# Kernel tuning notes

Measured on AMD Instinct MI355X. Metric: run time of the kernel, lower is better.

The kernel has to match this reference:

```python
import jax, jax.numpy as jnp
import numpy as np

N = 50000      # note nodes
IN = 128       # input feature dim
HID = 256      # GNN hidden dim
OH = 128       # hidden_dim // 2 after gnn.lin
CH = 64        # clf hidden (OH // 2)
OUT = 7        # cadence classes
E = 500000     # edges per relation
L = 3          # num_layers
T = 4          # edge types: onset, consecutive, during, rest
EPS = 1e-5


def _layernorm(h, g, b):
    mu = h.mean(-1, keepdims=True)
    var = h.var(-1, keepdims=True)
    return (h - mu) * jax.lax.rsqrt(var + EPS) * g + b


def setup_inputs() -> dict:
    key = jax.random.key(0)
    ks = jax.random.split(key, 24)
    s = 0.05
    inp = {
        "x": jax.random.normal(ks[0], (N, IN), jnp.float32),
        "edge_onset": jax.random.randint(ks[1], (2, E), 0, N),
        "edge_consecutive": jax.random.randint(ks[2], (2, E), 0, N),
        "edge_during": jax.random.randint(ks[3], (2, E), 0, N),
        "edge_rest": jax.random.randint(ks[4], (2, E), 0, N),
        # SAGEConv params: lin_l (with bias) on aggregated neighbors, lin_r (no bias) on self
        "Wl0": jax.random.normal(ks[5], (T, IN, HID), jnp.float32) * s,
        "bl0": jnp.zeros((T, HID), jnp.float32),
        "Wr0": jax.random.normal(ks[6], (T, IN, HID), jnp.float32) * s,
        "Wl": jax.random.normal(ks[7], (L - 1, T, HID, HID), jnp.float32) * s,
        "bl": jnp.zeros((L - 1, T, HID), jnp.float32),
        "Wr": jax.random.normal(ks[8], (L - 1, T, HID, HID), jnp.float32) * s,
        "lin_W": jax.random.normal(ks[9], (HID, OH), jnp.float32) * s,
        "lin_b": jnp.zeros((OH,), jnp.float32),
        "norm_g": jnp.ones((OH,), jnp.float32),
        "norm_b": jnp.zeros((OH,), jnp.float32),
        "pW1": jax.random.normal(ks[10], (OH, OH), jnp.float32) * s,
        "pb1": jnp.zeros((OH,), jnp.float32),
        "pln_g": jnp.ones((OH,), jnp.float32),
        "pln_b": jnp.zeros((OH,), jnp.float32),
        "pW2": jax.random.normal(ks[11], (OH, OH), jnp.float32) * s,
        "pb2": jnp.zeros((OH,), jnp.float32),
        "cW1": jax.random.normal(ks[12], (OH, CH), jnp.float32) * s,
        "cb1": jnp.zeros((CH,), jnp.float32),
        "bn_g": jnp.ones((CH,), jnp.float32),
        "bn_b": jnp.zeros((CH,), jnp.float32),
        "cW2": jax.random.normal(ks[13], (CH, OUT), jnp.float32) * s,
        "cb2": jnp.zeros((OUT,), jnp.float32),
    }
    return inp


def _mean_aggr(h, e):
    # SAGEConv mean aggregation: mean of source features per destination node
    src, dst = e[0], e[1]
    s = jax.ops.segment_sum(h[src], dst, num_segments=N)
    c = jax.ops.segment_sum(jnp.ones((e.shape[1], 1), h.dtype), dst, num_segments=N)
    return s / jnp.maximum(c, 1.0)


def _hetero_layer(h, edges, Wl_t, bl_t, Wr_t):
    # HeteroConv(aggr='sum'): sum SAGEConv outputs over edge types
    out = jnp.zeros((N, Wl_t.shape[-1]), h.dtype)
    for t in range(T):
        m = _mean_aggr(h, edges[t])
        out = out + m @ Wl_t[t] + bl_t[t] + h @ Wr_t[t]
    return jax.nn.relu(out)


def reference(x, edge_onset, edge_consecutive, edge_during, edge_rest,
              Wl0, bl0, Wr0, Wl, bl, Wr, lin_W, lin_b, norm_g, norm_b,
              pW1, pb1, pln_g, pln_b, pW2, pb2,
              cW1, cb1, bn_g, bn_b, cW2, cb2):
    edges = [edge_onset, edge_consecutive, edge_during, edge_rest]
    h = _hetero_layer(x, edges, Wl0, bl0, Wr0)
    for l in range(L - 1):
        h = _hetero_layer(h, edges, Wl[l], bl[l], Wr[l])
    h = h @ lin_W + lin_b  # [N, OH]

    # onset pooling: torch_scatter.scatter_mean(x[src], dst, out=x.clone())
    # -> (x + scatter_sum) / max(count, 1)
    src, dst = edge_onset[0], edge_onset[1]
    s = jax.ops.segment_sum(h[src], dst, num_segments=N)
    c = jax.ops.segment_sum(jnp.ones((E,), h.dtype), dst, num_segments=N)
    h = (h + s) / jnp.maximum(c, 1.0)[:, None]

    h = _layernorm(h, norm_g, norm_b)
    # pool_mlp (dropout = identity in eval)
    h = _layernorm(jax.nn.relu(h @ pW1 + pb1), pln_g, pln_b) @ pW2 + pb2
    # cad_clf: Linear -> ReLU -> BatchNorm1d (batch stats) -> Dropout(id) -> Linear
    z = jax.nn.relu(h @ cW1 + cb1)
    mu = z.mean(0)
    var = z.var(0)
    z = (z - mu) * jax.lax.rsqrt(var + EPS) * bn_g + bn_b
    logits = z @ cW2 + cb2
    return jax.nn.softmax(logits, axis=-1)
```

## Files before the change

### kernel.cpp

```cpp
#include <hip/hip_runtime.h>
#include <hip/hip_bf16.h>

#define NN    50000
#define ROWS  50048
#define DIN   128
#define DHID  256
#define DOH   128
#define DCH   64
#define DOUT  7
#define NE    500000
#define OFFS  50004
#define EPSV  1e-5f
#define LDAGG 1024

typedef unsigned int uint;
typedef unsigned short ushort;
using short8 = __attribute__((ext_vector_type(8))) short;
using f32x4  = __attribute__((ext_vector_type(4))) float;

__device__ inline float b2f(ushort u) {
    union { float f; uint i; } v; v.i = ((uint)u) << 16; return v.f;
}
__device__ inline ushort f2b(float f) {
    union { float f; uint u; } v; v.f = f;
    uint r = v.u + 0x7fff + ((v.u >> 16) & 1);
    return (ushort)(r >> 16);
}


__global__ void count_k(const int* __restrict__ d0, const int* __restrict__ d1,
                        const int* __restrict__ d2, const int* __restrict__ d3,
                        int* __restrict__ cnt) {
    int i = blockIdx.x * blockDim.x + threadIdx.x;
    if (i >= NE) return;
    int t = blockIdx.y;
    const int* d = (t == 0) ? d0 : (t == 1) ? d1 : (t == 2) ? d2 : d3;
    atomicAdd(&cnt[t * NN + d[i]], 1);
}

__global__ __launch_bounds__(1024)
void scan_k(const int* __restrict__ cnt, int* __restrict__ off) {
    const int* c = cnt + blockIdx.x * NN;
    int* o = off + blockIdx.x * OFFS;
    __shared__ int wsums[16];
    int lane = threadIdx.x & 63, wid = threadIdx.x >> 6;
    int carry = 0;
    for (int base = 0; base < NN; base += 1024) {
        int i = base + threadIdx.x;
        int v = (i < NN) ? c[i] : 0;
        int x = v;
        #pragma unroll
        for (int s = 1; s < 64; s <<= 1) {
            int t = __shfl_up(x, s);
            if (lane >= s) x += t;
        }
        if (lane == 63) wsums[wid] = x;
        __syncthreads();
        if (wid == 0) {
            int wv = (lane < 16) ? wsums[lane] : 0;
            #pragma unroll
            for (int s = 1; s < 16; s <<= 1) {
                int t = __shfl_up(wv, s);
                if (lane >= s) wv += t;
            }
            if (lane < 16) wsums[lane] = wv;
        }
        __syncthreads();
        int wprev = (wid == 0) ? 0 : wsums[wid - 1];
        if (i < NN) o[i] = carry + wprev + x - v;
        carry += wsums[15];
        __syncthreads();
    }
    if (threadIdx.x == 0) o[NN] = carry;
}

__global__ void copyoff_k(const int* __restrict__ off, int* __restrict__ cursor) {
    int i = blockIdx.x * blockDim.x + threadIdx.x;
    int t = blockIdx.y;
    if (i < NN) cursor[t * NN + i] = off[t * OFFS + i];
}

__global__ void scatter_k(const int* __restrict__ e0, const int* __restrict__ e1,
                          const int* __restrict__ e2, const int* __restrict__ e3,
                          int* __restrict__ cursor, int* __restrict__ sorted) {
    int i = blockIdx.x * blockDim.x + threadIdx.x;
    if (i >= NE) return;
    int t = blockIdx.y;
    const int* e = (t == 0) ? e0 : (t == 1) ? e1 : (t == 2) ? e2 : e3;
    int src = e[i], dst = e[NE + i];
    int p = atomicAdd(&cursor[t * NN + dst], 1);
    sorted[t * NE + p] = src;
}


__global__ void wprep_layer_k(const float* __restrict__ Wl, const float* __restrict__ Wr,
                              ushort* __restrict__ Bt, int Din) {
    int KA = 5 * Din;
    int K2 = 2 * KA;
    int i = blockIdx.x * 256 + threadIdx.x;
    if (i >= 256 * KA) return;
    int n = i / KA, k = i - n * KA;
    float v;
    if (k < 4 * Din) {
        int t = k / Din, c = k - t * Din;
        v = Wl[((size_t)t * Din + c) * 256 + n];
    } else {
        int c = k - 4 * Din;
        v = Wr[(size_t)c * 256 + n] + Wr[((size_t)Din + c) * 256 + n]
          + Wr[((size_t)2 * Din + c) * 256 + n] + Wr[((size_t)3 * Din + c) * 256 + n];
    }
    ushort hi = f2b(v);
    Bt[(size_t)n * K2 + k] = hi;
    Bt[(size_t)n * K2 + KA + k] = f2b(v - b2f(hi));
}

__global__ void wprep_t3_k(const float* __restrict__ W, ushort* __restrict__ Bt,
                           int N, int K) {
    int K3 = 3 * K;
    int i = blockIdx.x * 256 + threadIdx.x;
    if (i >= N * K3) return;
    int n = i / K3, k3 = i - n * K3;
    int k = (k3 < K) ? k3 : ((k3 < 2 * K) ? k3 - K : k3 - 2 * K);
    float v = W[(size_t)k * N + n];
    ushort hi = f2b(v);
    Bt[i] = (k3 < 2 * K) ? hi : f2b(v - b2f(hi));
}

__global__ void wsum_k(const float* __restrict__ W, float* __restrict__ wsum, int KN) {
    int i = blockIdx.x * blockDim.x + threadIdx.x;
    if (i < KN) wsum[i] = W[i] + W[KN + i] + W[2 * KN + i] + W[3 * KN + i];
}

__global__ void xconv_k(const float* __restrict__ x, ushort* __restrict__ aggbuf) {
    int i = blockIdx.x * 256 + threadIdx.x;
    if (i >= NN * DIN) return;
    int node = i >> 7, c = i & 127;
    aggbuf[(size_t)node * LDAGG + 512 + c] = f2b(x[i]);
}


template <int VE>
__global__ __launch_bounds__(256)
void aggrb_k(const ushort* __restrict__ hsrc, int hstride,
             const int* __restrict__ off, const int* __restrict__ sorted,
             ushort* __restrict__ out, int ostride) {
    int node = blockIdx.x * 4 + (threadIdx.x >> 6);
    if (node >= NN) return;
    int t = blockIdx.y;
    int l = threadIdx.x & 63;
    const int* of = off + (size_t)t * OFFS;
    const int* so = sorted + (size_t)t * NE;
    int s0 = of[node], s1 = of[node + 1];
    const ushort* hb = hsrc + (size_t)l * VE;
    float a0[VE] = {}, a1[VE] = {}, a2[VE] = {}, a3[VE] = {};
    int e = s0;
    if (VE == 2) {
        for (; e + 4 <= s1; e += 4) {
            uint vA = *(const uint*)(hb + (size_t)so[e]     * hstride);
            uint vB = *(const uint*)(hb + (size_t)so[e + 1] * hstride);
            uint vC = *(const uint*)(hb + (size_t)so[e + 2] * hstride);
            uint vD = *(const uint*)(hb + (size_t)so[e + 3] * hstride);
            a0[0] += b2f((ushort)vA); a0[1] += b2f((ushort)(vA >> 16));
            a1[0] += b2f((ushort)vB); a1[1] += b2f((ushort)(vB >> 16));
            a2[0] += b2f((ushort)vC); a2[1] += b2f((ushort)(vC >> 16));
            a3[0] += b2f((ushort)vD); a3[1] += b2f((ushort)(vD >> 16));
        }
        for (; e < s1; ++e) {
            uint v = *(const uint*)(hb + (size_t)so[e] * hstride);
            a0[0] += b2f((ushort)v); a0[1] += b2f((ushort)(v >> 16));
        }
    } else {
        for (; e + 4 <= s1; e += 4) {
            uint2 vA = *(const uint2*)(hb + (size_t)so[e]     * hstride);
            uint2 vB = *(const uint2*)(hb + (size_t)so[e + 1] * hstride);
            uint2 vC = *(const uint2*)(hb + (size_t)so[e + 2] * hstride);
            uint2 vD = *(const uint2*)(hb + (size_t)so[e + 3] * hstride);
            a0[0] += b2f((ushort)vA.x); a0[1] += b2f((ushort)(vA.x >> 16));
            a0[2] += b2f((ushort)vA.y); a0[3] += b2f((ushort)(vA.y >> 16));
            a1[0] += b2f((ushort)vB.x); a1[1] += b2f((ushort)(vB.x >> 16));
            a1[2] += b2f((ushort)vB.y); a1[3] += b2f((ushort)(vB.y >> 16));
            a2[0] += b2f((ushort)vC.x); a2[1] += b2f((ushort)(vC.x >> 16));
            a2[2] += b2f((ushort)vC.y); a2[3] += b2f((ushort)(vC.y >> 16));
            a3[0] += b2f((ushort)vD.x); a3[1] += b2f((ushort)(vD.x >> 16));
            a3[2] += b2f((ushort)vD.y); a3[3] += b2f((ushort)(vD.y >> 16));
        }
        for (; e < s1; ++e) {
            uint2 v = *(const uint2*)(hb + (size_t)so[e] * hstride);
            a0[0] += b2f((ushort)v.x); a0[1] += b2f((ushort)(v.x >> 16));
            a0[2] += b2f((ushort)v.y); a0[3] += b2f((ushort)(v.y >> 16));
        }
    }
    int deg = s1 - s0;
    float inv = 1.f / (float)(deg > 0 ? deg : 1);
    ushort* orow = out + (size_t)node * ostride + t * (64 * VE) + l * VE;
    if (VE == 2) {
        float r0 = (a0[0] + a1[0] + a2[0] + a3[0]) * inv;
        float r1 = (a0[1] + a1[1] + a2[1] + a3[1]) * inv;
        *(uint*)orow = (uint)f2b(r0) | ((uint)f2b(r1) << 16);
    } else {
        uint2 o;
        float r0 = (a0[0] + a1[0] + a2[0] + a3[0]) * inv;
        float r1 = (a0[1] + a1[1] + a2[1] + a3[1]) * inv;
        float r2 = (a0[2] + a1[2] + a2[2] + a3[2]) * inv;
        float r3 = (a0[3] + a1[3] + a2[3] + a3[3]) * inv;
        o.x = (uint)f2b(r0) | ((uint)f2b(r1) << 16);
        o.y = (uint)f2b(r2) | ((uint)f2b(r3) << 16);
        *(uint2*)orow = o;
    }
}


template <int BN, int NWN, bool RELU, int OMODE>
__global__ __launch_bounds__(128 * NWN)
void mgemm_k(const ushort* __restrict__ A, int lda,
             const ushort* __restrict__ A2, int lda2, int ksplit,
             const ushort* __restrict__ Bt, const float* __restrict__ bias,
             void* __restrict__ Cout, int ldc, int M, int K2, int KA) {
    constexpr int T = 128 * NWN;
    __shared__ ushort lsA[128 * 40];
    __shared__ ushort lsB[BN * 40];
    const int tid = threadIdx.x;
    const int l = tid & 63, wid = tid >> 6;
    const int wm = wid / NWN, wn = wid % NWN;
    const int row0 = blockIdx.x * 128;
    f32x4 acc[4][4] = {};
    for (int k0 = 0; k0 < K2; k0 += 32) {
        int kA = (k0 < KA) ? k0 : k0 - KA;
        const ushort* srcA;
        int lsrc;
        if (kA < ksplit) { srcA = A + kA; lsrc = lda; }
        else             { srcA = A2 + (kA - ksplit); lsrc = lda2; }
        #pragma unroll
        for (int q = 0; q < 512 / T; ++q) {
            int ch = tid + q * T;
            int r = ch >> 2, cb = ch & 3;
            short8 v = *(const short8*)(srcA + (size_t)(row0 + r) * lsrc + cb * 8);
            *(short8*)(lsA + r * 40 + cb * 8) = v;
        }
        #pragma unroll
        for (int q = 0; q < BN * 4 / T; ++q) {
            int ch = tid + q * T;
            int r = ch >> 2, cb = ch & 3;
            short8 v = *(const short8*)(Bt + (size_t)r * K2 + k0 + cb * 8);
            *(short8*)(lsB + r * 40 + cb * 8) = v;
        }
        __syncthreads();
        short8 af[4], bfr[4];
        #pragma unroll
        for (int fm = 0; fm < 4; ++fm)
            af[fm] = *(const short8*)(lsA + (wm * 64 + fm * 16 + (l & 15)) * 40 + (l >> 4) * 8);
        #pragma unroll
        for (int fn = 0; fn < 4; ++fn)
            bfr[fn] = *(const short8*)(lsB + (wn * 64 + fn * 16 + (l & 15)) * 40 + (l >> 4) * 8);
        #pragma unroll
        for (int fm = 0; fm < 4; ++fm)
            #pragma unroll
            for (int fn = 0; fn < 4; ++fn)
                acc[fm][fn] = __builtin_amdgcn_mfma_f32_16x16x32_bf16(
                    af[fm], bfr[fn], acc[fm][fn], 0, 0, 0);
        __syncthreads();
    }
    #pragma unroll
    for (int fm = 0; fm < 4; ++fm) {
        #pragma unroll
        for (int fn = 0; fn < 4; ++fn) {
            int col = wn * 64 + fn * 16 + (l & 15);
            float bv = bias[col];
            #pragma unroll
            for (int q = 0; q < 4; ++q) {
                int row = row0 + wm * 64 + fm * 16 + (l >> 4) * 4 + q;
                if (row < M) {
                    float v = acc[fm][fn][q] + bv;
                    if (RELU) v = fmaxf(v, 0.f);
                    if (OMODE == 0) {
                        ((float*)Cout)[(size_t)row * ldc + col] = v;
                    } else if (OMODE == 1) {
                        ((ushort*)Cout)[(size_t)row * ldc + col] = f2b(v);
                    } else {
                        ushort hv = f2b(v);
                        ((ushort*)Cout)[(size_t)row * ldc + col] = hv;
                        ((ushort*)Cout)[(size_t)row * ldc + col + BN] = f2b(v - b2f(hv));
                    }
                }
            }
        }
    }
}


__device__ inline float waveReduceSum(float v) {
    #pragma unroll
    for (int s = 32; s > 0; s >>= 1) v += __shfl_xor(v, s);
    return v;
}

__global__ __launch_bounds__(256)
void poolln_k(const float* __restrict__ hL, const int* __restrict__ off,
              const int* __restrict__ sorted, const float* __restrict__ g,
              const float* __restrict__ b, ushort* __restrict__ outS) {
    int node = blockIdx.x * 4 + (threadIdx.x >> 6);
    if (node >= NN) return;
    int l = threadIdx.x & 63;
    int s0 = off[node], s1 = off[node + 1];
    const float* hb = hL + (size_t)l * 2;
    float2 self = *(const float2*)(hb + (size_t)node * DOH);
    float a00 = 0, a01 = 0, a10 = 0, a11 = 0, a20 = 0, a21 = 0, a30 = 0, a31 = 0;
    int e = s0;
    for (; e + 4 <= s1; e += 4) {
        float2 vA = *(const float2*)(hb + (size_t)sorted[e]     * DOH);
        float2 vB = *(const float2*)(hb + (size_t)sorted[e + 1] * DOH);
        float2 vC = *(const float2*)(hb + (size_t)sorted[e + 2] * DOH);
        float2 vD = *(const float2*)(hb + (size_t)sorted[e + 3] * DOH);
        a00 += vA.x; a01 += vA.y; a10 += vB.x; a11 += vB.y;
        a20 += vC.x; a21 += vC.y; a30 += vD.x; a31 += vD.y;
    }
    for (; e < s1; ++e) {
        float2 v = *(const float2*)(hb + (size_t)sorted[e] * DOH);
        a00 += v.x; a01 += v.y;
    }
    int deg = s1 - s0;
    float inv = 1.f / (float)(deg > 0 ? deg : 1);
    float v0 = (self.x + a00 + a10 + a20 + a30) * inv;
    float v1 = (self.y + a01 + a11 + a21 + a31) * inv;
    float mean = waveReduceSum(v0 + v1) * (1.f / DOH);
    float ex2  = waveReduceSum(v0 * v0 + v1 * v1) * (1.f / DOH);
    float rst = rsqrtf(ex2 - mean * mean + EPSV);
    float o0 = (v0 - mean) * rst * g[2 * l] + b[2 * l];
    float o1 = (v1 - mean) * rst * g[2 * l + 1] + b[2 * l + 1];
    ushort h0 = f2b(o0), h1 = f2b(o1);
    ushort l0 = f2b(o0 - b2f(h0)), l1 = f2b(o1 - b2f(h1));
    ushort* row = outS + (size_t)node * 256;
    *(uint*)(row + 2 * l)       = (uint)h0 | ((uint)h1 << 16);
    *(uint*)(row + 128 + 2 * l) = (uint)l0 | ((uint)l1 << 16);
}

__global__ __launch_bounds__(256)
void lns_k(ushort* __restrict__ hS, const float* __restrict__ g,
           const float* __restrict__ b) {
    int node = blockIdx.x * 4 + (threadIdx.x >> 6);
    if (node >= NN) return;
    int l = threadIdx.x & 63;
    ushort* row = hS + (size_t)node * 256;
    uint hh = *(uint*)(row + 2 * l);
    uint ll = *(uint*)(row + 128 + 2 * l);
    float v0 = b2f((ushort)hh) + b2f((ushort)ll);
    float v1 = b2f((ushort)(hh >> 16)) + b2f((ushort)(ll >> 16));
    float mean = waveReduceSum(v0 + v1) * (1.f / DOH);
    float ex2  = waveReduceSum(v0 * v0 + v1 * v1) * (1.f / DOH);
    float rst = rsqrtf(ex2 - mean * mean + EPSV);
    float o0 = (v0 - mean) * rst * g[2 * l] + b[2 * l];
    float o1 = (v1 - mean) * rst * g[2 * l + 1] + b[2 * l + 1];
    ushort h0 = f2b(o0), h1 = f2b(o1);
    ushort lo0 = f2b(o0 - b2f(h0)), lo1 = f2b(o1 - b2f(h1));
    *(uint*)(row + 2 * l)       = (uint)h0 | ((uint)h1 << 16);
    *(uint*)(row + 128 + 2 * l) = (uint)lo0 | ((uint)lo1 << 16);
}


__global__ __launch_bounds__(256)
void bnstat_k(const float* __restrict__ z, float* __restrict__ sums, int M) {
    int col = threadIdx.x & 63;
    int rgrp = threadIdx.x >> 6;
    float s = 0.f, s2 = 0.f;
    for (int r = blockIdx.x * 4 + rgrp; r < M; r += gridDim.x * 4) {
        float v = z[(size_t)r * DCH + col];
        s += v; s2 += v * v;
    }
    __shared__ float sh[2][4][64];
    sh[0][rgrp][col] = s;
    sh[1][rgrp][col] = s2;
    __syncthreads();
    if (rgrp == 0) {
        s  = sh[0][0][col] + sh[0][1][col] + sh[0][2][col] + sh[0][3][col];
        s2 = sh[1][0][col] + sh[1][1][col] + sh[1][2][col] + sh[1][3][col];
        atomicAdd(&sums[col], s);
        atomicAdd(&sums[64 + col], s2);
    }
}

__global__ __launch_bounds__(256)
void final_k(const float* __restrict__ z, const float* __restrict__ sums,
             const float* __restrict__ bn_g, const float* __restrict__ bn_b,
             const float* __restrict__ cW2, const float* __restrict__ cb2,
             float* __restrict__ out, int M) {
    int row = blockIdx.x * 4 + (threadIdx.x >> 6);
    int lane = threadIdx.x & 63;
    if (row >= M) return;
    float zv = z[(size_t)row * DCH + lane];
    float mean = sums[lane] * (1.f / M);
    float var = sums[64 + lane] * (1.f / M) - mean * mean;
    float zb = (zv - mean) * rsqrtf(var + EPSV) * bn_g[lane] + bn_b[lane];
    float logit[DOUT];
    #pragma unroll
    for (int o = 0; o < DOUT; ++o) {
        float p = zb * cW2[lane * DOUT + o];
        #pragma unroll
        for (int s = 32; s > 0; s >>= 1) p += __shfl_xor(p, s);
        logit[o] = p + cb2[o];
    }
    float mx = logit[0];
    #pragma unroll
    for (int o = 1; o < DOUT; ++o) mx = fmaxf(mx, logit[o]);
    float den = 0.f;
    #pragma unroll
    for (int o = 0; o < DOUT; ++o) { logit[o] = expf(logit[o] - mx); den += logit[o]; }
    float inv = 1.f / den;
    if (lane == 0) {
        #pragma unroll
        for (int o = 0; o < DOUT; ++o) out[(size_t)row * DOUT + o] = logit[o] * inv;
    }
}


extern "C" void kernel_launch(void* const* d_in, const int* in_sizes, int n_in,
                              void* d_out, int out_size, void* d_ws, size_t ws_size,
                              hipStream_t stream) {
    const float* x     = (const float*)d_in[0];
    const int* eptr[4] = {(const int*)d_in[1], (const int*)d_in[2],
                          (const int*)d_in[3], (const int*)d_in[4]};
    const float* Wl0   = (const float*)d_in[5];
    const float* bl0   = (const float*)d_in[6];
    const float* Wr0   = (const float*)d_in[7];
    const float* Wl    = (const float*)d_in[8];
    const float* bl    = (const float*)d_in[9];
    const float* Wr    = (const float*)d_in[10];
    const float* lin_W = (const float*)d_in[11];
    const float* lin_b = (const float*)d_in[12];
    const float* nrm_g = (const float*)d_in[13];
    const float* nrm_b = (const float*)d_in[14];
    const float* pW1   = (const float*)d_in[15];
    const float* pb1   = (const float*)d_in[16];
    const float* pln_g = (const float*)d_in[17];
    const float* pln_b = (const float*)d_in[18];
    const float* pW2   = (const float*)d_in[19];
    const float* pb2   = (const float*)d_in[20];
    const float* cW1   = (const float*)d_in[21];
    const float* cb1   = (const float*)d_in[22];
    const float* bn_g  = (const float*)d_in[23];
    const float* bn_b  = (const float*)d_in[24];
    const float* cW2   = (const float*)d_in[25];
    const float* cb2   = (const float*)d_in[26];

    size_t wo = 0;
    auto alloc = [&](size_t bytes) -> void* {
        void* p = (char*)d_ws + wo;
        wo += (bytes + 255) & ~(size_t)255;
        return p;
    };
    int* off      = (int*)alloc(4 * OFFS * sizeof(int));
    int* cursor   = (int*)alloc(4 * NN * sizeof(int));
    int* sorted   = (int*)alloc(4 * NE * sizeof(int));
    ushort* WBt   = (ushort*)alloc((size_t)256 * 2560 * 2);
    ushort* BtLin = (ushort*)alloc((size_t)128 * 768 * 2);
    ushort* BtP1  = (ushort*)alloc((size_t)128 * 384 * 2);
    ushort* BtP2  = (ushort*)alloc((size_t)128 * 384 * 2);
    ushort* BtC1  = (ushort*)alloc((size_t)64 * 384 * 2);
    float* bsum   = (float*)alloc(256 * sizeof(float));
    float* bnsum  = (float*)alloc(128 * sizeof(float));
    ushort* aggbuf = (ushort*)alloc((size_t)ROWS * LDAGG * 2);
    ushort* hc1   = (ushort*)alloc((size_t)ROWS * 256 * 2);
    ushort* hc2   = (ushort*)alloc((size_t)ROWS * 256 * 2);

    float*  hL  = (float*)hc1;
    ushort* hPs = hc2;
    ushort* hQs = aggbuf;
    ushort* hRs = (ushort*)((char*)aggbuf + ((size_t)32 << 20));
    float*  z   = (float*)((char*)aggbuf + ((size_t)64 << 20));

    const int EB = (NE + 255) / 256;
    const int GX = (NN + 127) / 128;
    const int AGG = (NN + 3) / 4;

    hipMemsetAsync(cursor, 0, 4 * NN * sizeof(int), stream);
    count_k<<<dim3(EB, 4), 256, 0, stream>>>(eptr[0] + NE, eptr[1] + NE,
                                             eptr[2] + NE, eptr[3] + NE, cursor);
    scan_k<<<4, 1024, 0, stream>>>(cursor, off);
    copyoff_k<<<dim3((NN + 255) / 256, 4), 256, 0, stream>>>(off, cursor);
    scatter_k<<<dim3(EB, 4), 256, 0, stream>>>(eptr[0], eptr[1], eptr[2], eptr[3],
                                               cursor, sorted);

    xconv_k<<<(NN * DIN + 255) / 256, 256, 0, stream>>>(x, aggbuf);

    wprep_layer_k<<<(256 * 640 + 255) / 256, 256, 0, stream>>>(Wl0, Wr0, WBt, DIN);
    wsum_k<<<1, 256, 0, stream>>>(bl0, bsum, DHID);
    aggrb_k<2><<<dim3(AGG, 4), 256, 0, stream>>>(aggbuf + 512, LDAGG, off, sorted,
                                                 aggbuf, LDAGG);
    mgemm_k<256, 4, true, 1><<<GX, 512, 0, stream>>>(
        aggbuf, LDAGG, aggbuf, LDAGG, 640, WBt, bsum, (void*)hc1, 256, NN, 1280, 640);

    for (int l = 1; l < 3; ++l) {
        const float* WlP = Wl + (size_t)(l - 1) * 4 * DHID * DHID;
        const float* blP = bl + (size_t)(l - 1) * 4 * DHID;
        const float* WrP = Wr + (size_t)(l - 1) * 4 * DHID * DHID;
        ushort* hin = (l == 1) ? hc1 : hc2;
        wprep_layer_k<<<(256 * 1280 + 255) / 256, 256, 0, stream>>>(WlP, WrP, WBt, DHID);
        wsum_k<<<1, 256, 0, stream>>>(blP, bsum, DHID);
        aggrb_k<4><<<dim3(AGG, 4), 256, 0, stream>>>(hin, 256, off, sorted,
                                                     aggbuf, LDAGG);
        if (l == 1)
            mgemm_k<256, 4, true, 1><<<GX, 512, 0, stream>>>(
                aggbuf, LDAGG, hin, 256, 1024, WBt, bsum, (void*)hc2, 256, NN, 2560, 1280);
        else
            mgemm_k<256, 4, true, 2><<<GX, 512, 0, stream>>>(
                aggbuf, LDAGG, hin, 256, 1024, WBt, bsum, (void*)aggbuf, LDAGG, NN, 2560, 1280);
    }

    wprep_t3_k<<<(128 * 768 + 255) / 256, 256, 0, stream>>>(lin_W, BtLin, DOH, DHID);
    mgemm_k<128, 2, false, 0><<<GX, 256, 0, stream>>>(
        aggbuf, LDAGG, aggbuf, LDAGG, 512, BtLin, lin_b, (void*)hL, DOH, NN, 768, 512);

    poolln_k<<<AGG, 256, 0, stream>>>(hL, off, sorted, nrm_g, nrm_b, hPs);

    wprep_t3_k<<<(128 * 384 + 255) / 256, 256, 0, stream>>>(pW1, BtP1, DOH, DOH);
    mgemm_k<128, 2, true, 2><<<GX, 256, 0, stream>>>(
        hPs, 256, hPs, 256, 256, BtP1, pb1, (void*)hQs, 256, NN, 384, 256);
    lns_k<<<AGG, 256, 0, stream>>>(hQs, pln_g, pln_b);
    wprep_t3_k<<<(128 * 384 + 255) / 256, 256, 0, stream>>>(pW2, BtP2, DOH, DOH);
    mgemm_k<128, 2, false, 2><<<GX, 256, 0, stream>>>(
        hQs, 256, hQs, 256, 256, BtP2, pb2, (void*)hRs, 256, NN, 384, 256);

    wprep_t3_k<<<(64 * 384 + 255) / 256, 256, 0, stream>>>(cW1, BtC1, DCH, DOH);
    mgemm_k<64, 1, true, 0><<<GX, 128, 0, stream>>>(
        hRs, 256, hRs, 256, 256, BtC1, cb1, (void*)z, DCH, NN, 384, 256);
    hipMemsetAsync(bnsum, 0, 128 * sizeof(float), stream);
    bnstat_k<<<256, 256, 0, stream>>>(z, bnsum, NN);
    final_k<<<AGG, 256, 0, stream>>>(z, bnsum, bn_g, bn_b, cW2, cb2,
                                     (float*)d_out, NN);
}
```

Before: 1.277 ms.

## Fuse neighbor mean aggregation into per-layer SAGE GEMM kernel and drop copyoff

Each of the three hetero SAGE layers now runs one kernel. It first gathers and averages neighbor features for its 128-row tile across all four relations into aggbuf, then runs the bf16 MFMA GEMM on those same rows. This removes a separate aggregation launch per layer and lets the GEMM read freshly written aggregates, likely from L2. The scan kernel also writes the cursor array directly, which removes the copyoff kernel. In exchange the gather phase no longer overlaps with the MFMA phase inside a block, and gather parallelism is now bound to the GEMM grid of large 512-thread blocks.

After: 1.521 ms. +19.1%, slower.

```diff
diff --git a/kernel.cpp b/kernel.cpp
--- a/kernel.cpp
+++ b/kernel.cpp
@@ -39,9 +39,11 @@
 }
 
 __global__ __launch_bounds__(1024)
-void scan_k(const int* __restrict__ cnt, int* __restrict__ off) {
+void scan_k(const int* __restrict__ cnt, int* __restrict__ off,
+            int* __restrict__ cursor) {
     const int* c = cnt + blockIdx.x * NN;
     int* o = off + blockIdx.x * OFFS;
+    int* cu = cursor + blockIdx.x * NN;
     __shared__ int wsums[16];
     int lane = threadIdx.x & 63, wid = threadIdx.x >> 6;
     int carry = 0;
@@ -67,17 +69,15 @@
         }
         __syncthreads();
         int wprev = (wid == 0) ? 0 : wsums[wid - 1];
-        if (i < NN) o[i] = carry + wprev + x - v;
+        if (i < NN) {
+            int ex = carry + wprev + x - v;
+            o[i] = ex;
+            cu[i] = ex;
+        }
         carry += wsums[15];
         __syncthreads();
     }
     if (threadIdx.x == 0) o[NN] = carry;
-}
-
-__global__ void copyoff_k(const int* __restrict__ off, int* __restrict__ cursor) {
-    int i = blockIdx.x * blockDim.x + threadIdx.x;
-    int t = blockIdx.y;
-    if (i < NN) cursor[t * NN + i] = off[t * OFFS + i];
 }
 
 __global__ void scatter_k(const int* __restrict__ e0, const int* __restrict__ e1,
@@ -139,73 +139,149 @@
 }
 
 
-template <int VE>
-__global__ __launch_bounds__(256)
-void aggrb_k(const ushort* __restrict__ hsrc, int hstride,
-             const int* __restrict__ off, const int* __restrict__ sorted,
-             ushort* __restrict__ out, int ostride) {
-    int node = blockIdx.x * 4 + (threadIdx.x >> 6);
-    if (node >= NN) return;
-    int t = blockIdx.y;
-    int l = threadIdx.x & 63;
-    const int* of = off + (size_t)t * OFFS;
-    const int* so = sorted + (size_t)t * NE;
-    int s0 = of[node], s1 = of[node + 1];
-    const ushort* hb = hsrc + (size_t)l * VE;
-    float a0[VE] = {}, a1[VE] = {}, a2[VE] = {}, a3[VE] = {};
-    int e = s0;
-    if (VE == 2) {
-        for (; e + 4 <= s1; e += 4) {
-            uint vA = *(const uint*)(hb + (size_t)so[e]     * hstride);
-            uint vB = *(const uint*)(hb + (size_t)so[e + 1] * hstride);
-            uint vC = *(const uint*)(hb + (size_t)so[e + 2] * hstride);
-            uint vD = *(const uint*)(hb + (size_t)so[e + 3] * hstride);
-            a0[0] += b2f((ushort)vA); a0[1] += b2f((ushort)(vA >> 16));
-            a1[0] += b2f((ushort)vB); a1[1] += b2f((ushort)(vB >> 16));
-            a2[0] += b2f((ushort)vC); a2[1] += b2f((ushort)(vC >> 16));
-            a3[0] += b2f((ushort)vD); a3[1] += b2f((ushort)(vD >> 16));
-        }
-        for (; e < s1; ++e) {
-            uint v = *(const uint*)(hb + (size_t)so[e] * hstride);
-            a0[0] += b2f((ushort)v); a0[1] += b2f((ushort)(v >> 16));
-        }
-    } else {
-        for (; e + 4 <= s1; e += 4) {
-            uint2 vA = *(const uint2*)(hb + (size_t)so[e]     * hstride);
-            uint2 vB = *(const uint2*)(hb + (size_t)so[e + 1] * hstride);
-            uint2 vC = *(const uint2*)(hb + (size_t)so[e + 2] * hstride);
-            uint2 vD = *(const uint2*)(hb + (size_t)so[e + 3] * hstride);
-            a0[0] += b2f((ushort)vA.x); a0[1] += b2f((ushort)(vA.x >> 16));
-            a0[2] += b2f((ushort)vA.y); a0[3] += b2f((ushort)(vA.y >> 16));
-            a1[0] += b2f((ushort)vB.x); a1[1] += b2f((ushort)(vB.x >> 16));
-            a1[2] += b2f((ushort)vB.y); a1[3] += b2f((ushort)(vB.y >> 16));
-            a2[0] += b2f((ushort)vC.x); a2[1] += b2f((ushort)(vC.x >> 16));
-            a2[2] += b2f((ushort)vC.y); a2[3] += b2f((ushort)(vC.y >> 16));
-            a3[0] += b2f((ushort)vD.x); a3[1] += b2f((ushort)(vD.x >> 16));
-            a3[2] += b2f((ushort)vD.y); a3[3] += b2f((ushort)(vD.y >> 16));
-        }
-        for (; e < s1; ++e) {
-            uint2 v = *(const uint2*)(hb + (size_t)so[e] * hstride);
-            a0[0] += b2f((ushort)v.x); a0[1] += b2f((ushort)(v.x >> 16));
-            a0[2] += b2f((ushort)v.y); a0[3] += b2f((ushort)(v.y >> 16));
-        }
-    }
-    int deg = s1 - s0;
-    float inv = 1.f / (float)(deg > 0 ? deg : 1);
-    ushort* orow = out + (size_t)node * ostride + t * (64 * VE) + l * VE;
-    if (VE == 2) {
-        float r0 = (a0[0] + a1[0] + a2[0] + a3[0]) * inv;
-        float r1 = (a0[1] + a1[1] + a2[1] + a3[1]) * inv;
-        *(uint*)orow = (uint)f2b(r0) | ((uint)f2b(r1) << 16);
-    } else {
-        uint2 o;
-        float r0 = (a0[0] + a1[0] + a2[0] + a3[0]) * inv;
-        float r1 = (a0[1] + a1[1] + a2[1] + a3[1]) * inv;
-        float r2 = (a0[2] + a1[2] + a2[2] + a3[2]) * inv;
-        float r3 = (a0[3] + a1[3] + a2[3] + a3[3]) * inv;
-        o.x = (uint)f2b(r0) | ((uint)f2b(r1) << 16);
-        o.y = (uint)f2b(r2) | ((uint)f2b(r3) << 16);
-        *(uint2*)orow = o;
+template <int VE, bool RELU, int OMODE>
+__global__ __launch_bounds__(512)
+void flayer_k(const ushort* __restrict__ hsrc, int hstride,
+              const int* __restrict__ off, const int* __restrict__ sorted,
+              ushort* __restrict__ aggbuf,
+              const ushort* __restrict__ A2, int lda2, int ksplit,
+              const ushort* __restrict__ Bt, const float* __restrict__ bias,
+              void* __restrict__ Cout, int ldc, int M, int K2, int KA) {
+    constexpr int BN = 256;
+    constexpr int T = 512;
+    __shared__ ushort lsA[128 * 40];
+    __shared__ ushort lsB[BN * 40];
+    const int tid = threadIdx.x;
+    const int l = tid & 63, wid = tid >> 6;
+    const int row0 = blockIdx.x * 128;
+
+    for (int task = wid; task < 512; task += 8) {
+        int node = row0 + (task >> 2);
+        int t = task & 3;
+        if (node >= M) continue;
+        const int* of = off + (size_t)t * OFFS;
+        const int* so = sorted + (size_t)t * NE;
+        int s0 = of[node], s1 = of[node + 1];
+        const ushort* hb = hsrc + (size_t)l * VE;
+        float a0[VE] = {}, a1[VE] = {}, a2v[VE] = {}, a3[VE] = {};
+        int e = s0;
+        if (VE == 2) {
+            for (; e + 4 <= s1; e += 4) {
+                uint vA = *(const uint*)(hb + (size_t)so[e]     * hstride);
+                uint vB = *(const uint*)(hb + (size_t)so[e + 1] * hstride);
+                uint vC = *(const uint*)(hb + (size_t)so[e + 2] * hstride);
+                uint vD = *(const uint*)(hb + (size_t)so[e + 3] * hstride);
+                a0[0] += b2f((ushort)vA); a0[1] += b2f((ushort)(vA >> 16));
+                a1[0] += b2f((ushort)vB); a1[1] += b2f((ushort)(vB >> 16));
+                a2v[0] += b2f((ushort)vC); a2v[1] += b2f((ushort)(vC >> 16));
+                a3[0] += b2f((ushort)vD); a3[1] += b2f((ushort)(vD >> 16));
+            }
+            for (; e < s1; ++e) {
+                uint v = *(const uint*)(hb + (size_t)so[e] * hstride);
+                a0[0] += b2f((ushort)v); a0[1] += b2f((ushort)(v >> 16));
+            }
+        } else {
+            for (; e + 4 <= s1; e += 4) {
+                uint2 vA = *(const uint2*)(hb + (size_t)so[e]     * hstride);
+                uint2 vB = *(const uint2*)(hb + (size_t)so[e + 1] * hstride);
+                uint2 vC = *(const uint2*)(hb + (size_t)so[e + 2] * hstride);
+                uint2 vD = *(const uint2*)(hb + (size_t)so[e + 3] * hstride);
+                a0[0] += b2f((ushort)vA.x); a0[1] += b2f((ushort)(vA.x >> 16));
+                a0[2] += b2f((ushort)vA.y); a0[3] += b2f((ushort)(vA.y >> 16));
+                a1[0] += b2f((ushort)vB.x); a1[1] += b2f((ushort)(vB.x >> 16));
+                a1[2] += b2f((ushort)vB.y); a1[3] += b2f((ushort)(vB.y >> 16));
+                a2v[0] += b2f((ushort)vC.x); a2v[1] += b2f((ushort)(vC.x >> 16));
+                a2v[2] += b2f((ushort)vC.y); a2v[3] += b2f((ushort)(vC.y >> 16));
+                a3[0] += b2f((ushort)vD.x); a3[1] += b2f((ushort)(vD.x >> 16));
+                a3[2] += b2f((ushort)vD.y); a3[3] += b2f((ushort)(vD.y >> 16));
+            }
+            for (; e < s1; ++e) {
+                uint2 v = *(const uint2*)(hb + (size_t)so[e] * hstride);
+                a0[0] += b2f((ushort)v.x); a0[1] += b2f((ushort)(v.x >> 16));
+                a0[2] += b2f((ushort)v.y); a0[3] += b2f((ushort)(v.y >> 16));
+            }
+        }
+        int deg = s1 - s0;
+        float inv = 1.f / (float)(deg > 0 ? deg : 1);
+        ushort* orow = aggbuf + (size_t)node * LDAGG + t * (64 * VE) + l * VE;
+        if (VE == 2) {
+            float r0 = (a0[0] + a1[0] + a2v[0] + a3[0]) * inv;
+            float r1 = (a0[1] + a1[1] + a2v[1] + a3[1]) * inv;
+            *(uint*)orow = (uint)f2b(r0) | ((uint)f2b(r1) << 16);
+        } else {
+            uint2 o;
+            float r0 = (a0[0] + a1[0] + a2v[0] + a3[0]) * inv;
+            float r1 = (a0[1] + a1[1] + a2v[1] + a3[1]) * inv;
+            float r2 = (a0[2] + a1[2] + a2v[2] + a3[2]) * inv;
+            float r3 = (a0[3] + a1[3] + a2v[3] + a3[3]) * inv;
+            o.x = (uint)f2b(r0) | ((uint)f2b(r1) << 16);
+            o.y = (uint)f2b(r2) | ((uint)f2b(r3) << 16);
+            *(uint2*)orow = o;
+        }
+    }
+    __syncthreads();
+
+    const int wm = wid / 4, wn = wid % 4;
+    f32x4 acc[4][4] = {};
+    for (int k0 = 0; k0 < K2; k0 += 32) {
+        int kA = (k0 < KA) ? k0 : k0 - KA;
+        const ushort* srcA;
+        int lsrc;
+        if (kA < ksplit) { srcA = aggbuf + kA; lsrc = LDAGG; }
+        else             { srcA = A2 + (kA - ksplit); lsrc = lda2; }
+        {
+            int ch = tid;
+            int r = ch >> 2, cb = ch & 3;
+            short8 v = *(const short8*)(srcA + (size_t)(row0 + r) * lsrc + cb * 8);
+            *(short8*)(lsA + r * 40 + cb * 8) = v;
+        }
+        #pragma unroll
+        for (int q = 0; q < 2; ++q) {
+            int ch = tid + q * T;
+            int r = ch >> 2, cb = ch & 3;
+            short8 v = *(const short8*)(Bt + (size_t)r * K2 + k0 + cb * 8);
+            *(short8*)(lsB + r * 40 + cb * 8) = v;
+        }
+        __syncthreads();
+        short8 af[4], bfr[4];
+        #pragma unroll
+        for (int fm = 0; fm < 4; ++fm)
+            af[fm] = *(const short8*)(lsA + (wm * 64 + fm * 16 + (l & 15)) * 40 + (l >> 4) * 8);
+        #pragma unroll
+        for (int fn = 0; fn < 4; ++fn)
+            bfr[fn] = *(const short8*)(lsB + (wn * 64 + fn * 16 + (l & 15)) * 40 + (l >> 4) * 8);
+        #pragma unroll
+        for (int fm = 0; fm < 4; ++fm)
+            #pragma unroll
+            for (int fn = 0; fn < 4; ++fn)
+                acc[fm][fn] = __builtin_amdgcn_mfma_f32_16x16x32_bf16(
+                    af[fm], bfr[fn], acc[fm][fn], 0, 0, 0);
+        __syncthreads();
+    }
+    #pragma unroll
+    for (int fm = 0; fm < 4; ++fm) {
+        #pragma unroll
+        for (int fn = 0; fn < 4; ++fn) {
+            int col = wn * 64 + fn * 16 + (l & 15);
+            float bv = bias[col];
+            #pragma unroll
+            for (int q = 0; q < 4; ++q) {
+                int row = row0 + wm * 64 + fm * 16 + (l >> 4) * 4 + q;
+                if (row < M) {
+                    float v = acc[fm][fn][q] + bv;
+                    if (RELU) v = fmaxf(v, 0.f);
+                    if (OMODE == 0) {
+                        ((float*)Cout)[(size_t)row * ldc + col] = v;
+                    } else if (OMODE == 1) {
+                        ((ushort*)Cout)[(size_t)row * ldc + col] = f2b(v);
+                    } else {
+                        ushort hv = f2b(v);
+                        ((ushort*)Cout)[(size_t)row * ldc + col] = hv;
+                        ((ushort*)Cout)[(size_t)row * ldc + col + BN] = f2b(v - b2f(hv));
+                    }
+                }
+            }
+        }
     }
 }
 
@@ -474,8 +550,7 @@
     hipMemsetAsync(cursor, 0, 4 * NN * sizeof(int), stream);
     count_k<<<dim3(EB, 4), 256, 0, stream>>>(eptr[0] + NE, eptr[1] + NE,
                                              eptr[2] + NE, eptr[3] + NE, cursor);
-    scan_k<<<4, 1024, 0, stream>>>(cursor, off);
-    copyoff_k<<<dim3((NN + 255) / 256, 4), 256, 0, stream>>>(off, cursor);
+    scan_k<<<4, 1024, 0, stream>>>(cursor, off, cursor);
     scatter_k<<<dim3(EB, 4), 256, 0, stream>>>(eptr[0], eptr[1], eptr[2], eptr[3],
                                                cursor, sorted);
 
@@ -483,10 +558,9 @@
 
     wprep_layer_k<<<(256 * 640 + 255) / 256, 256, 0, stream>>>(Wl0, Wr0, WBt, DIN);
     wsum_k<<<1, 256, 0, stream>>>(bl0, bsum, DHID);
-    aggrb_k<2><<<dim3(AGG, 4), 256, 0, stream>>>(aggbuf + 512, LDAGG, off, sorted,
-                                                 aggbuf, LDAGG);
-    mgemm_k<256, 4, true, 1><<<GX, 512, 0, stream>>>(
-        aggbuf, LDAGG, aggbuf, LDAGG, 640, WBt, bsum, (void*)hc1, 256, NN, 1280, 640);
+    flayer_k<2, true, 1><<<GX, 512, 0, stream>>>(
+        aggbuf + 512, LDAGG, off, sorted, aggbuf,
+        aggbuf, LDAGG, 640, WBt, bsum, (void*)hc1, 256, NN, 1280, 640);
 
     for (int l = 1; l < 3; ++l) {
         const float* WlP = Wl + (size_t)(l - 1) * 4 * DHID * DHID;
@@ -495,14 +569,14 @@
         ushort* hin = (l == 1) ? hc1 : hc2;
         wprep_layer_k<<<(256 * 1280 + 255) / 256, 256, 0, stream>>>(WlP, WrP, WBt, DHID);
         wsum_k<<<1, 256, 0, stream>>>(blP, bsum, DHID);
-        aggrb_k<4><<<dim3(AGG, 4), 256, 0, stream>>>(hin, 256, off, sorted,
-                                                     aggbuf, LDAGG);
         if (l == 1)
-            mgemm_k<256, 4, true, 1><<<GX, 512, 0, stream>>>(
-                aggbuf, LDAGG, hin, 256, 1024, WBt, bsum, (void*)hc2, 256, NN, 2560, 1280);
+            flayer_k<4, true, 1><<<GX, 512, 0, stream>>>(
+                hin, 256, off, sorted, aggbuf,
+                hin, 256, 1024, WBt, bsum, (void*)hc2, 256, NN, 2560, 1280);
         else
-            mgemm_k<256, 4, true, 2><<<GX, 512, 0, stream>>>(
-                aggbuf, LDAGG, hin, 256, 1024, WBt, bsum, (void*)aggbuf, LDAGG, NN, 2560, 1280);
+            flayer_k<4, true, 2><<<GX, 512, 0, stream>>>(
+                hin, 256, off, sorted, aggbuf,
+                hin, 256, 1024, WBt, bsum, (void*)aggbuf, LDAGG, NN, 2560, 1280);
     }
 
     wprep_t3_k<<<(128 * 768 + 255) / 256, 256, 0, stream>>>(lin_W, BtLin, DOH, DHID);
```

## Widen gather loads to 16-byte vectors with edge-split lanes in aggregation kernels

Applied to the files above, without the earlier changes.

Rewrites the neighbor-aggregation kernels so each lane loads 16 bytes (8 bf16) per gathered row instead of 4 or 8 bytes. Subgroups of the wave handle different edges in parallel and are combined with cross-lane shuffles. The same scheme is applied to the pooling+layernorm kernel using float4 loads. The separate offset-to-cursor copy kernel is folded into the scan kernel, which removes one launch. The goal is fewer, wider memory transactions per edge and more memory-level parallelism, at the cost of extra shuffles and idle lanes on the final store.

Measured after the change: 1.254 ms. Within noise of the previous version (-1.8%).

```diff
diff --git a/kernel.cpp b/kernel.cpp
--- a/kernel.cpp
+++ b/kernel.cpp
@@ -26,6 +26,15 @@
     uint r = v.u + 0x7fff + ((v.u >> 16) & 1);
     return (ushort)(r >> 16);
 }
+__device__ inline uint packb(float a, float b) {
+    return (uint)f2b(a) | ((uint)f2b(b) << 16);
+}
+
+#define ACC8(A, V) do { \
+    A[0] += b2f((ushort)(V.x)); A[1] += b2f((ushort)((V.x) >> 16)); \
+    A[2] += b2f((ushort)(V.y)); A[3] += b2f((ushort)((V.y) >> 16)); \
+    A[4] += b2f((ushort)(V.z)); A[5] += b2f((ushort)((V.z) >> 16)); \
+    A[6] += b2f((ushort)(V.w)); A[7] += b2f((ushort)((V.w) >> 16)); } while (0)
 
 
 __global__ void count_k(const int* __restrict__ d0, const int* __restrict__ d1,
@@ -39,9 +48,11 @@
 }
 
 __global__ __launch_bounds__(1024)
-void scan_k(const int* __restrict__ cnt, int* __restrict__ off) {
+void scan_k(const int* __restrict__ cnt, int* __restrict__ off,
+            int* __restrict__ cursor) {
     const int* c = cnt + blockIdx.x * NN;
     int* o = off + blockIdx.x * OFFS;
+    int* cu = cursor + blockIdx.x * NN;
     __shared__ int wsums[16];
     int lane = threadIdx.x & 63, wid = threadIdx.x >> 6;
     int carry = 0;
@@ -67,17 +78,15 @@
         }
         __syncthreads();
         int wprev = (wid == 0) ? 0 : wsums[wid - 1];
-        if (i < NN) o[i] = carry + wprev + x - v;
+        if (i < NN) {
+            int ex = carry + wprev + x - v;
+            o[i] = ex;
+            cu[i] = ex;
+        }
         carry += wsums[15];
         __syncthreads();
     }
     if (threadIdx.x == 0) o[NN] = carry;
-}
-
-__global__ void copyoff_k(const int* __restrict__ off, int* __restrict__ cursor) {
-    int i = blockIdx.x * blockDim.x + threadIdx.x;
-    int t = blockIdx.y;
-    if (i < NN) cursor[t * NN + i] = off[t * OFFS + i];
 }
 
 __global__ void scatter_k(const int* __restrict__ e0, const int* __restrict__ e1,
@@ -139,73 +148,89 @@
 }
 
 
-template <int VE>
 __global__ __launch_bounds__(256)
-void aggrb_k(const ushort* __restrict__ hsrc, int hstride,
-             const int* __restrict__ off, const int* __restrict__ sorted,
-             ushort* __restrict__ out, int ostride) {
+void aggrb128_k(const ushort* __restrict__ hsrc,
+                const int* __restrict__ off, const int* __restrict__ sorted,
+                ushort* __restrict__ out) {
     int node = blockIdx.x * 4 + (threadIdx.x >> 6);
     if (node >= NN) return;
     int t = blockIdx.y;
     int l = threadIdx.x & 63;
+    int quad = l >> 4, li = l & 15;
     const int* of = off + (size_t)t * OFFS;
     const int* so = sorted + (size_t)t * NE;
     int s0 = of[node], s1 = of[node + 1];
-    const ushort* hb = hsrc + (size_t)l * VE;
-    float a0[VE] = {}, a1[VE] = {}, a2[VE] = {}, a3[VE] = {};
-    int e = s0;
-    if (VE == 2) {
-        for (; e + 4 <= s1; e += 4) {
-            uint vA = *(const uint*)(hb + (size_t)so[e]     * hstride);
-            uint vB = *(const uint*)(hb + (size_t)so[e + 1] * hstride);
-            uint vC = *(const uint*)(hb + (size_t)so[e + 2] * hstride);
-            uint vD = *(const uint*)(hb + (size_t)so[e + 3] * hstride);
-            a0[0] += b2f((ushort)vA); a0[1] += b2f((ushort)(vA >> 16));
-            a1[0] += b2f((ushort)vB); a1[1] += b2f((ushort)(vB >> 16));
-            a2[0] += b2f((ushort)vC); a2[1] += b2f((ushort)(vC >> 16));
-            a3[0] += b2f((ushort)vD); a3[1] += b2f((ushort)(vD >> 16));
-        }
-        for (; e < s1; ++e) {
-            uint v = *(const uint*)(hb + (size_t)so[e] * hstride);
-            a0[0] += b2f((ushort)v); a0[1] += b2f((ushort)(v >> 16));
-        }
-    } else {
-        for (; e + 4 <= s1; e += 4) {
-            uint2 vA = *(const uint2*)(hb + (size_t)so[e]     * hstride);
-            uint2 vB = *(const uint2*)(hb + (size_t)so[e + 1] * hstride);
-            uint2 vC = *(const uint2*)(hb + (size_t)so[e + 2] * hstride);
-            uint2 vD = *(const uint2*)(hb + (size_t)so[e + 3] * hstride);
-            a0[0] += b2f((ushort)vA.x); a0[1] += b2f((ushort)(vA.x >> 16));
-            a0[2] += b2f((ushort)vA.y); a0[3] += b2f((ushort)(vA.y >> 16));
-            a1[0] += b2f((ushort)vB.x); a1[1] += b2f((ushort)(vB.x >> 16));
-            a1[2] += b2f((ushort)vB.y); a1[3] += b2f((ushort)(vB.y >> 16));
-            a2[0] += b2f((ushort)vC.x); a2[1] += b2f((ushort)(vC.x >> 16));
-            a2[2] += b2f((ushort)vC.y); a2[3] += b2f((ushort)(vC.y >> 16));
-            a3[0] += b2f((ushort)vD.x); a3[1] += b2f((ushort)(vD.x >> 16));
-            a3[2] += b2f((ushort)vD.y); a3[3] += b2f((ushort)(vD.y >> 16));
-        }
-        for (; e < s1; ++e) {
-            uint2 v = *(const uint2*)(hb + (size_t)so[e] * hstride);
-            a0[0] += b2f((ushort)v.x); a0[1] += b2f((ushort)(v.x >> 16));
-            a0[2] += b2f((ushort)v.y); a0[3] += b2f((ushort)(v.y >> 16));
-        }
+    const ushort* hb = hsrc + (size_t)li * 8;
+    float a0[8] = {}, a1[8] = {};
+    int e = s0 + quad;
+    for (; e + 4 < s1; e += 8) {
+        uint4 v = *(const uint4*)(hb + (size_t)so[e] * LDAGG);
+        uint4 w = *(const uint4*)(hb + (size_t)so[e + 4] * LDAGG);
+        ACC8(a0, v);
+        ACC8(a1, w);
+    }
+    if (e < s1) {
+        uint4 v = *(const uint4*)(hb + (size_t)so[e] * LDAGG);
+        ACC8(a0, v);
+    }
+    #pragma unroll
+    for (int j = 0; j < 8; ++j) {
+        a0[j] += a1[j];
+        a0[j] += __shfl_xor(a0[j], 16);
+        a0[j] += __shfl_xor(a0[j], 32);
     }
     int deg = s1 - s0;
     float inv = 1.f / (float)(deg > 0 ? deg : 1);
-    ushort* orow = out + (size_t)node * ostride + t * (64 * VE) + l * VE;
-    if (VE == 2) {
-        float r0 = (a0[0] + a1[0] + a2[0] + a3[0]) * inv;
-        float r1 = (a0[1] + a1[1] + a2[1] + a3[1]) * inv;
-        *(uint*)orow = (uint)f2b(r0) | ((uint)f2b(r1) << 16);
-    } else {
-        uint2 o;
-        float r0 = (a0[0] + a1[0] + a2[0] + a3[0]) * inv;
-        float r1 = (a0[1] + a1[1] + a2[1] + a3[1]) * inv;
-        float r2 = (a0[2] + a1[2] + a2[2] + a3[2]) * inv;
-        float r3 = (a0[3] + a1[3] + a2[3] + a3[3]) * inv;
-        o.x = (uint)f2b(r0) | ((uint)f2b(r1) << 16);
-        o.y = (uint)f2b(r2) | ((uint)f2b(r3) << 16);
-        *(uint2*)orow = o;
+    if (quad == 0) {
+        uint4 o;
+        o.x = packb(a0[0] * inv, a0[1] * inv);
+        o.y = packb(a0[2] * inv, a0[3] * inv);
+        o.z = packb(a0[4] * inv, a0[5] * inv);
+        o.w = packb(a0[6] * inv, a0[7] * inv);
+        *(uint4*)(out + (size_t)node * LDAGG + t * 128 + li * 8) = o;
+    }
+}
+
+
+__global__ __launch_bounds__(256)
+void aggrb256_k(const ushort* __restrict__ hsrc,
+                const int* __restrict__ off, const int* __restrict__ sorted,
+                ushort* __restrict__ out) {
+    int node = blockIdx.x * 4 + (threadIdx.x >> 6);
+    if (node >= NN) return;
+    int t = blockIdx.y;
+    int l = threadIdx.x & 63;
+    int half = l >> 5, li = l & 31;
+    const int* of = off + (size_t)t * OFFS;
+    const int* so = sorted + (size_t)t * NE;
+    int s0 = of[node], s1 = of[node + 1];
+    const ushort* hb = hsrc + (size_t)li * 8;
+    float a0[8] = {}, a1[8] = {};
+    int e = s0 + half;
+    for (; e + 2 < s1; e += 4) {
+        uint4 v = *(const uint4*)(hb + (size_t)so[e] * 256);
+        uint4 w = *(const uint4*)(hb + (size_t)so[e + 2] * 256);
+        ACC8(a0, v);
+        ACC8(a1, w);
+    }
+    if (e < s1) {
+        uint4 v = *(const uint4*)(hb + (size_t)so[e] * 256);
+        ACC8(a0, v);
+    }
+    #pragma unroll
+    for (int j = 0; j < 8; ++j) {
+        a0[j] += a1[j];
+        a0[j] += __shfl_xor(a0[j], 32);
+    }
+    int deg = s1 - s0;
+    float inv = 1.f / (float)(deg > 0 ? deg : 1);
+    if (half == 0) {
+        uint4 o;
+        o.x = packb(a0[0] * inv, a0[1] * inv);
+        o.y = packb(a0[2] * inv, a0[3] * inv);
+        o.z = packb(a0[4] * inv, a0[5] * inv);
+        o.w = packb(a0[6] * inv, a0[7] * inv);
+        *(uint4*)(out + (size_t)node * LDAGG + t * 256 + li * 8) = o;
     }
 }
 
@@ -301,37 +326,53 @@
     int node = blockIdx.x * 4 + (threadIdx.x >> 6);
     if (node >= NN) return;
     int l = threadIdx.x & 63;
+    int half = l >> 5, li = l & 31;
     int s0 = off[node], s1 = off[node + 1];
-    const float* hb = hL + (size_t)l * 2;
-    float2 self = *(const float2*)(hb + (size_t)node * DOH);
-    float a00 = 0, a01 = 0, a10 = 0, a11 = 0, a20 = 0, a21 = 0, a30 = 0, a31 = 0;
-    int e = s0;
-    for (; e + 4 <= s1; e += 4) {
-        float2 vA = *(const float2*)(hb + (size_t)sorted[e]     * DOH);
-        float2 vB = *(const float2*)(hb + (size_t)sorted[e + 1] * DOH);
-        float2 vC = *(const float2*)(hb + (size_t)sorted[e + 2] * DOH);
-        float2 vD = *(const float2*)(hb + (size_t)sorted[e + 3] * DOH);
-        a00 += vA.x; a01 += vA.y; a10 += vB.x; a11 += vB.y;
-        a20 += vC.x; a21 += vC.y; a30 += vD.x; a31 += vD.y;
-    }
-    for (; e < s1; ++e) {
-        float2 v = *(const float2*)(hb + (size_t)sorted[e] * DOH);
-        a00 += v.x; a01 += v.y;
+    const float* hb = hL + (size_t)li * 4;
+    float4 self = *(const float4*)(hb + (size_t)node * DOH);
+    float a0[4] = {}, a1[4] = {};
+    int e = s0 + half;
+    for (; e + 2 < s1; e += 4) {
+        float4 v = *(const float4*)(hb + (size_t)sorted[e] * DOH);
+        float4 w = *(const float4*)(hb + (size_t)sorted[e + 2] * DOH);
+        a0[0] += v.x; a0[1] += v.y; a0[2] += v.z; a0[3] += v.w;
+        a1[0] += w.x; a1[1] += w.y; a1[2] += w.z; a1[3] += w.w;
+    }
+    if (e < s1) {
+        float4 v = *(const float4*)(hb + (size_t)sorted[e] * DOH);
+        a0[0] += v.x; a0[1] += v.y; a0[2] += v.z; a0[3] += v.w;
+    }
+    #pragma unroll
+    for (int j = 0; j < 4; ++j) {
+        a0[j] += a1[j];
+        a0[j] += __shfl_xor(a0[j], 32);
     }
     int deg = s1 - s0;
     float inv = 1.f / (float)(deg > 0 ? deg : 1);
-    float v0 = (self.x + a00 + a10 + a20 + a30) * inv;
-    float v1 = (self.y + a01 + a11 + a21 + a31) * inv;
-    float mean = waveReduceSum(v0 + v1) * (1.f / DOH);
-    float ex2  = waveReduceSum(v0 * v0 + v1 * v1) * (1.f / DOH);
+    float v0 = (self.x + a0[0]) * inv;
+    float v1 = (self.y + a0[1]) * inv;
+    float v2 = (self.z + a0[2]) * inv;
+    float v3 = (self.w + a0[3]) * inv;
+    float mean = waveReduceSum(v0 + v1 + v2 + v3) * (1.f / (2 * DOH));
+    float ex2  = waveReduceSum(v0 * v0 + v1 * v1 + v2 * v2 + v3 * v3) * (1.f / (2 * DOH));
     float rst = rsqrtf(ex2 - mean * mean + EPSV);
-    float o0 = (v0 - mean) * rst * g[2 * l] + b[2 * l];
-    float o1 = (v1 - mean) * rst * g[2 * l + 1] + b[2 * l + 1];
-    ushort h0 = f2b(o0), h1 = f2b(o1);
-    ushort l0 = f2b(o0 - b2f(h0)), l1 = f2b(o1 - b2f(h1));
-    ushort* row = outS + (size_t)node * 256;
-    *(uint*)(row + 2 * l)       = (uint)h0 | ((uint)h1 << 16);
-    *(uint*)(row + 128 + 2 * l) = (uint)l0 | ((uint)l1 << 16);
+    float4 gv = *(const float4*)(g + li * 4);
+    float4 bv = *(const float4*)(b + li * 4);
+    float o0 = (v0 - mean) * rst * gv.x + bv.x;
+    float o1 = (v1 - mean) * rst * gv.y + bv.y;
+    float o2 = (v2 - mean) * rst * gv.z + bv.z;
+    float o3 = (v3 - mean) * rst * gv.w + bv.w;
+    if (half == 0) {
+        ushort* row = outS + (size_t)node * 256;
+        ushort h0 = f2b(o0), h1 = f2b(o1), h2 = f2b(o2), h3 = f2b(o3);
+        uint2 hi, lo;
+        hi.x = (uint)h0 | ((uint)h1 << 16);
+        hi.y = (uint)h2 | ((uint)h3 << 16);
+        lo.x = packb(o0 - b2f(h0), o1 - b2f(h1));
+        lo.y = packb(o2 - b2f(h2), o3 - b2f(h3));
+        *(uint2*)(row + li * 4)       = hi;
+        *(uint2*)(row + 128 + li * 4) = lo;
+    }
 }
 
 __global__ __launch_bounds__(256)
@@ -474,8 +515,7 @@
     hipMemsetAsync(cursor, 0, 4 * NN * sizeof(int), stream);
     count_k<<<dim3(EB, 4), 256, 0, stream>>>(eptr[0] + NE, eptr[1] + NE,
                                              eptr[2] + NE, eptr[3] + NE, cursor);
-    scan_k<<<4, 1024, 0, stream>>>(cursor, off);
-    copyoff_k<<<dim3((NN + 255) / 256, 4), 256, 0, stream>>>(off, cursor);
+    scan_k<<<4, 1024, 0, stream>>>(cursor, off, cursor);
     scatter_k<<<dim3(EB, 4), 256, 0, stream>>>(eptr[0], eptr[1], eptr[2], eptr[3],
                                                cursor, sorted);
 
@@ -483,8 +523,7 @@
 
     wprep_layer_k<<<(256 * 640 + 255) / 256, 256, 0, stream>>>(Wl0, Wr0, WBt, DIN);
     wsum_k<<<1, 256, 0, stream>>>(bl0, bsum, DHID);
-    aggrb_k<2><<<dim3(AGG, 4), 256, 0, stream>>>(aggbuf + 512, LDAGG, off, sorted,
-                                                 aggbuf, LDAGG);
+    aggrb128_k<<<dim3(AGG, 4), 256, 0, stream>>>(aggbuf + 512, off, sorted, aggbuf);
     mgemm_k<256, 4, true, 1><<<GX, 512, 0, stream>>>(
         aggbuf, LDAGG, aggbuf, LDAGG, 640, WBt, bsum, (void*)hc1, 256, NN, 1280, 640);
 
@@ -495,8 +534,7 @@
         ushort* hin = (l == 1) ? hc1 : hc2;
         wprep_layer_k<<<(256 * 1280 + 255) / 256, 256, 0, stream>>>(WlP, WrP, WBt, DHID);
         wsum_k<<<1, 256, 0, stream>>>(blP, bsum, DHID);
-        aggrb_k<4><<<dim3(AGG, 4), 256, 0, stream>>>(hin, 256, off, sorted,
-                                                     aggbuf, LDAGG);
+        aggrb256_k<<<dim3(AGG, 4), 256, 0, stream>>>(hin, off, sorted, aggbuf);
         if (l == 1)
             mgemm_k<256, 4, true, 1><<<GX, 512, 0, stream>>>(
                 aggbuf, LDAGG, hin, 256, 1024, WBt, bsum, (void*)hc2, 256, NN, 2560, 1280);
```
